# Kernel tuning notes

Measured on AMD Instinct MI355X. Metric: run time of the kernel, lower is better.

The kernel has to match this reference:

```python
import jax, jax.numpy as jnp
import numpy as np
import math

B, S, H, NH = 8, 1024, 1024, 16
DH = H // NH


def _ln(x, g, b, eps=1e-5):
    m = x.mean(-1, keepdims=True)
    v = ((x - m) ** 2).mean(-1, keepdims=True)
    return (x - m) / jnp.sqrt(v + eps) * g + b


def _attn(qx, kx, vx, wq, bq, wk, bk, wv, bv, wo, bo, mask):
    b = qx.shape[0]
    def heads(t, w, bias):
        return (t @ w + bias).reshape(b, -1, NH, DH).transpose(0, 2, 1, 3)
    q, k, v = heads(qx, wq, bq), heads(kx, wk, bk), heads(vx, wv, bv)
    corr = jnp.einsum('bhqd,bhkd->bhqk', q, k) / math.sqrt(DH)  # [B,NH,Sq,Sk]
    corr = jnp.where(mask[:, None, :, None] == 0, -1e9, corr)  # mask per query row
    p = jax.nn.softmax(corr, axis=-1)
    o = jnp.einsum('bhqk,bhkd->bhqd', p, v).transpose(0, 2, 1, 3).reshape(b, -1, H)
    return o @ wo + bo


def setup_inputs() -> dict:
    key = jax.random.key(0)
    ks = jax.random.split(key, 16)
    d = {}
    d['x'] = jax.random.normal(ks[0], (B, S, H), jnp.float32)
    d['h'] = jax.random.normal(ks[1], (B, S, H), jnp.float32)
    d['mask'] = jnp.ones((B, S), jnp.int32)
    wnames = ['sa_wq', 'sa_wk', 'sa_wv', 'sa_wo', 'ca_wq', 'ca_wk', 'ca_wv', 'ca_wo', 'ff_w1', 'ff_w2']
    for i, n in enumerate(wnames):
        d[n] = jax.random.normal(ks[2 + i], (H, H), jnp.float32) * 0.02
    for n in ['sa_bq', 'sa_bk', 'sa_bv', 'sa_bo', 'ca_bq', 'ca_bk', 'ca_bv', 'ca_bo', 'ff_b1', 'ff_b2']:
        d[n] = jnp.zeros((H,), jnp.float32)
    for n in ['ln1', 'ln2', 'ln3', 'lnh', 'ff_ln']:
        d[n + '_g'] = jnp.ones((H,), jnp.float32)
        d[n + '_b'] = jnp.zeros((H,), jnp.float32)
    return d


def reference(x, h, mask, ln1_g, ln1_b, ln2_g, ln2_b, ln3_g, ln3_b, lnh_g, lnh_b,
              sa_wq, sa_bq, sa_wk, sa_bk, sa_wv, sa_bv, sa_wo, sa_bo,
              ca_wq, ca_bq, ca_wk, ca_bk, ca_wv, ca_bv, ca_wo, ca_bo,
              ff_w1, ff_b1, ff_w2, ff_b2, ff_ln_g, ff_ln_b):
    # self-attention block (pre-LN, residual)
    xn = _ln(x, ln1_g, ln1_b)
    hidden_in = _attn(xn, xn, xn, sa_wq, sa_bq, sa_wk, sa_bk, sa_wv, sa_bv, sa_wo, sa_bo, mask) + x
    # cross-attention block
    mid_n = _ln(hidden_in, ln2_g, ln2_b)
    hn = _ln(h, lnh_g, lnh_b)
    hidden_mid = _attn(mid_n, hn, hn, ca_wq, ca_bq, ca_wk, ca_bk, ca_wv, ca_bv, ca_wo, ca_bo, mask) + hidden_in
    # position-wise FFN (Conv1d k=1 == pointwise linear) with its own LN+residual
    y = _ln(hidden_mid, ln3_g, ln3_b)
    ff = jax.nn.relu(y @ ff_w1 + ff_b1) @ ff_w2 + ff_b2
    ffo = _ln(ff + y, ff_ln_g, ff_ln_b)
    return ffo + hidden_mid
```

## Files before the change

kernel.cpp:

```cpp
#include <hip/hip_runtime.h>

typedef unsigned short u16;
typedef unsigned int u32;
typedef float f32x4 __attribute__((ext_vector_type(4)));
typedef float f32x16 __attribute__((ext_vector_type(16)));
typedef __bf16 bf16x8 __attribute__((ext_vector_type(8)));

#define MFMA16(a, b, c) __builtin_amdgcn_mfma_f32_16x16x32_bf16(a, b, c, 0, 0, 0)
#define MFMA32(a, b, c) __builtin_amdgcn_mfma_f32_32x32x16_bf16(a, b, c, 0, 0, 0)
#define PLSWAP(x, y) asm volatile("v_permlane32_swap_b32 %0, %1" : "+v"(x), "+v"(y))
#define CFENCE() asm volatile("" ::: "memory")
#define BAR()                         \
    {                                 \
        CFENCE();                     \
        __builtin_amdgcn_s_barrier(); \
        CFENCE();                     \
    }
#define WAITV(n) asm volatile("s_waitcnt vmcnt(" #n ")" ::: "memory")

__device__ __forceinline__ u16 f2b(float f) {
    u32 u = __builtin_bit_cast(u32, f);
    u += 0x7fffu + ((u >> 16) & 1u);
    return (u16)(u >> 16);
}

__device__ __forceinline__ float b2f(u16 v) {
    u32 u = ((u32)v) << 16;
    return __builtin_bit_cast(float, u);
}

__device__ __forceinline__ u32 pk2(float a, float b) {
    union { u32 u; __bf16 h[2]; } r;
    r.h[0] = (__bf16)a; r.h[1] = (__bf16)b;
    return r.u;
}

__device__ __forceinline__ void gload16(const u16* g, u16* l) {
    __builtin_amdgcn_global_load_lds((const __attribute__((address_space(1))) void*)g,
                                     (__attribute__((address_space(3))) void*)l, 16, 0, 0);
}

struct W10 { const float* p[10]; };
__global__ __launch_bounds__(256) void tcvt_k(W10 wp, u16* __restrict__ WT0) {
    const float* __restrict__ Wm = wp.p[blockIdx.z];
    u16* __restrict__ WT = WT0 + (size_t)blockIdx.z * 1048576;
    __shared__ float t[32][33];
    int bx = blockIdx.x, by = blockIdx.y;
    int tx = threadIdx.x, ty = threadIdx.y;
#pragma unroll
    for (int j = 0; j < 32; j += 8)
        t[ty + j][tx] = Wm[(size_t)(by * 32 + ty + j) * 1024 + bx * 32 + tx];
    __syncthreads();
#pragma unroll
    for (int j = 0; j < 32; j += 8)
        WT[(size_t)(bx * 32 + ty + j) * 1024 + by * 32 + tx] = f2b(t[tx][ty + j]);
}

template <int MODE>
__global__ __launch_bounds__(256) void ln_k(const float* __restrict__ in1, const float* __restrict__ in2,
                                            const float* __restrict__ gg, const float* __restrict__ bb,
                                            const float* __restrict__ post,
                                            float* __restrict__ of, u16* __restrict__ ob) {
    int row = blockIdx.x, tid = threadIdx.x;
    size_t base = (size_t)row * 1024 + tid * 4;
    float4 x = *(const float4*)(in1 + base);
    if constexpr (MODE & 1) {
        float4 x2 = *(const float4*)(in2 + base);
        x.x += x2.x; x.y += x2.y; x.z += x2.z; x.w += x2.w;
    }
    float s1 = x.x + x.y + x.z + x.w;
    float s2 = x.x * x.x + x.y * x.y + x.z * x.z + x.w * x.w;
#pragma unroll
    for (int m = 32; m >= 1; m >>= 1) { s1 += __shfl_xor(s1, m); s2 += __shfl_xor(s2, m); }
    __shared__ float r1[4], r2[4];
    int lane = tid & 63, w = tid >> 6;
    if (lane == 0) { r1[w] = s1; r2[w] = s2; }
    __syncthreads();
    s1 = r1[0] + r1[1] + r1[2] + r1[3];
    s2 = r2[0] + r2[1] + r2[2] + r2[3];
    float mean = s1 * (1.0f / 1024.0f);
    float var = s2 * (1.0f / 1024.0f) - mean * mean;
    float rstd = rsqrtf(var + 1e-5f);
    float4 gv = *(const float4*)(gg + tid * 4);
    float4 bv = *(const float4*)(bb + tid * 4);
    float y0 = (x.x - mean) * rstd * gv.x + bv.x;
    float y1 = (x.y - mean) * rstd * gv.y + bv.y;
    float y2 = (x.z - mean) * rstd * gv.z + bv.z;
    float y3 = (x.w - mean) * rstd * gv.w + bv.w;
    if constexpr (MODE & 2) {
        float o0 = y0, o1 = y1, o2 = y2, o3 = y3;
        if constexpr (MODE & 8) {
            float4 p = *(const float4*)(post + base);
            o0 += p.x; o1 += p.y; o2 += p.z; o3 += p.w;
        }
        float4 o; o.x = o0; o.y = o1; o.z = o2; o.w = o3;
        *(float4*)(of + base) = o;
    }
    if constexpr (MODE & 4) {
        uint2 pk;
        pk.x = (u32)f2b(y0) | ((u32)f2b(y1) << 16);
        pk.y = (u32)f2b(y2) | ((u32)f2b(y3) << 16);
        *(uint2*)(ob + base) = pk;
    }
}

__global__ __launch_bounds__(256) void ln2x_k(const float* __restrict__ inA, const float* __restrict__ gA,
                                              const float* __restrict__ bA, u16* __restrict__ obA,
                                              const float* __restrict__ inB, const float* __restrict__ gB,
                                              const float* __restrict__ bB, u16* __restrict__ obB) {
    int sel = blockIdx.x >> 13;
    int row = blockIdx.x & 8191;
    const float* in1 = sel ? inB : inA;
    const float* gg = sel ? gB : gA;
    const float* bb = sel ? bB : bA;
    u16* ob = sel ? obB : obA;
    int tid = threadIdx.x;
    size_t base = (size_t)row * 1024 + tid * 4;
    float4 x = *(const float4*)(in1 + base);
    float s1 = x.x + x.y + x.z + x.w;
    float s2 = x.x * x.x + x.y * x.y + x.z * x.z + x.w * x.w;
#pragma unroll
    for (int m = 32; m >= 1; m >>= 1) { s1 += __shfl_xor(s1, m); s2 += __shfl_xor(s2, m); }
    __shared__ float r1[4], r2[4];
    int lane = tid & 63, w = tid >> 6;
    if (lane == 0) { r1[w] = s1; r2[w] = s2; }
    __syncthreads();
    s1 = r1[0] + r1[1] + r1[2] + r1[3];
    s2 = r2[0] + r2[1] + r2[2] + r2[3];
    float mean = s1 * (1.0f / 1024.0f);
    float var = s2 * (1.0f / 1024.0f) - mean * mean;
    float rstd = rsqrtf(var + 1e-5f);
    float4 gv = *(const float4*)(gg + tid * 4);
    float4 bv = *(const float4*)(bb + tid * 4);
    uint2 pk;
    pk.x = pk2((x.x - mean) * rstd * gv.x + bv.x, (x.y - mean) * rstd * gv.y + bv.y);
    pk.y = pk2((x.z - mean) * rstd * gv.z + bv.z, (x.w - mean) * rstd * gv.w + bv.w);
    *(uint2*)(ob + base) = pk;
}

template <int EPI, int NBN, int VSEG>
__global__ __launch_bounds__(512) void gemm512_k(const u16* __restrict__ A, int lda,
                                                 const u16* __restrict__ WT,
                                                 const float* __restrict__ b0, const float* __restrict__ b1,
                                                 const float* __restrict__ b2,
                                                 float sc0, float sc1, float sc2,
                                                 const float* __restrict__ res,
                                                 void* __restrict__ outp, int ldc,
                                                 u16* __restrict__ vt) {
    constexpr int ASZ = 8192;
    constexpr int SLOT = ASZ + 4096;
    __shared__ u16 lds[3 * SLOT];
    u16* ldsb = &lds[0];

    int id = blockIdx.x;
    constexpr int NWG = 32 * NBN;
    constexpr int CPX = NWG / 8;
    int swz = (id & 7) * CPX + (id >> 3);
    int bm = swz / NBN, bn = swz % NBN;
    const int m0 = bm * 256, n0 = bn * 128;
    int tid = threadIdx.x, lane = tid & 63, w = tid >> 6;
    int col = lane & 15, fg = lane >> 4;
    int wr = w >> 1, wc = w & 1;

    int swzL = ((col * 32) + fg * 8) ^ ((col >> 1) << 3);
    int aoff0 = wr * 64 * 32 + swzL;
    int boff0 = ASZ + wc * 64 * 32 + swzL;

    int r = tid >> 2, g = tid & 3;
    int gr = r ^ ((r >> 3) & 1);
    int gc = g ^ ((r >> 1) & 3);
    const u16* pA = A + (size_t)(m0 + gr) * lda + gc * 8;
    const u16* pB = WT + (size_t)(n0 + gr) * 1024 + gc * 8;

#define STGA(t2, snO)                                                                       \
    {                                                                                       \
        gload16(pA + (size_t)(t2) * 32, ldsb + (snO) + w * 512);                            \
        gload16(pA + (size_t)(t2) * 32 + (size_t)128 * lda, ldsb + (snO) + 4096 + w * 512); \
    }
#define STGB(t2, snO)                                                   \
    {                                                                   \
        gload16(pB + (size_t)(t2) * 32, ldsb + (snO) + ASZ + w * 512);  \
    }

    f32x4 acc[4][4];
#pragma unroll
    for (int m = 0; m < 4; m++)
#pragma unroll
        for (int n = 0; n < 4; n++) acc[m][n] = (f32x4){0.f, 0.f, 0.f, 0.f};

    STGA(0, 0); STGB(0, 0);
    STGA(1, SLOT); STGB(1, SLOT);
    WAITV(3);
    BAR();

    int sc = 0, sn = 2;
    for (int t = 0; t < 32; ++t) {
        int sCur = sc * SLOT, sNxt = sn * SLOT;
        bf16x8 a0[4], bfv[2];
#pragma unroll
        for (int m = 0; m < 4; m++) a0[m] = *(const bf16x8*)&ldsb[sCur + aoff0 + m * 512];
#pragma unroll
        for (int n = 0; n < 2; n++) bfv[n] = *(const bf16x8*)&ldsb[sCur + boff0 + n * 512];
        if (t < 30) STGA(t + 2, sNxt);
        BAR();
        __builtin_amdgcn_s_setprio(1);
#pragma unroll
        for (int m = 0; m < 4; m++)
#pragma unroll
            for (int n = 0; n < 2; n++) acc[m][n] = MFMA16(a0[m], bfv[n], acc[m][n]);
        __builtin_amdgcn_s_setprio(0);
        BAR();
        bf16x8 b2[2];
#pragma unroll
        for (int n = 0; n < 2; n++) b2[n] = *(const bf16x8*)&ldsb[sCur + boff0 + (n + 2) * 512];
        if (t < 30) STGB(t + 2, sNxt);
        BAR();
        __builtin_amdgcn_s_setprio(1);
#pragma unroll
        for (int m = 0; m < 4; m++)
#pragma unroll
            for (int n = 0; n < 2; n++) acc[m][n + 2] = MFMA16(a0[m], b2[n], acc[m][n + 2]);
        __builtin_amdgcn_s_setprio(0);
        if (t < 30) { WAITV(3); } else if (t == 30) { WAITV(0); }
        BAR();
        sc = (sc == 2) ? 0 : sc + 1;
        sn = (sn == 2) ? 0 : sn + 1;
    }
#undef STGA
#undef STGB

    int seg = n0 >> 10;
    const float* bp = (seg == 0) ? b0 : (seg == 1 ? b1 : b2);
    float sg = (seg == 0) ? sc0 : (seg == 1 ? sc1 : sc2);
    int nseg = n0 & 1023;
    float bv[4];
#pragma unroll
    for (int n = 0; n < 4; n++) bv[n] = bp[nseg + wc * 64 + n * 16 + col];

    if constexpr (VSEG >= 0) {
        if (seg == VSEG) {
            int chl = wc * 64 + col;
            int keyl = wr * 64 + fg * 4;
#pragma unroll
            for (int m = 0; m < 4; m++)
#pragma unroll
                for (int n = 0; n < 4; n++) {
                    uint2 pk;
                    pk.x = pk2(acc[m][n][0] + bv[n], acc[m][n][1] + bv[n]);
                    pk.y = pk2(acc[m][n][2] + bv[n], acc[m][n][3] + bv[n]);
                    *(uint2*)&ldsb[(chl + n * 16) * 264 + keyl + m * 16] = pk;
                }
            BAR();
            int bidx = m0 >> 10;
            int keyg = m0 & 1023;
            int rowt = tid >> 5, cht = tid & 31;
#pragma unroll
            for (int p = 0; p < 8; p++) {
                int ch = p * 16 + rowt;
                uint4 v4 = *(const uint4*)&ldsb[ch * 264 + cht * 8];
                *(uint4*)(vt + ((size_t)(bidx * 1024 + nseg + ch) << 10) + keyg + cht * 8) = v4;
            }
            return;
        }
    }
#pragma unroll
    for (int m = 0; m < 4; m++) {
#pragma unroll
        for (int rr = 0; rr < 4; rr++) {
            int row = m0 + wr * 64 + m * 16 + fg * 4 + rr;
#pragma unroll
            for (int n = 0; n < 4; n++) {
                int c = n0 + wc * 64 + n * 16 + col;
                size_t idx = (size_t)row * ldc + c;
                float v = (acc[m][n][rr] + bv[n]) * sg;
                if constexpr (EPI == 0) ((u16*)outp)[idx] = f2b(v);
                else if constexpr (EPI == 1) ((u16*)outp)[idx] = f2b(fmaxf(v, 0.f));
                else if constexpr (EPI == 2) ((float*)outp)[idx] = v + res[idx];
            }
        }
    }
}

template <int EPI, int NBN>
__global__ __launch_bounds__(256) void gemm256_k(const u16* __restrict__ A, int lda,
                                                 const u16* __restrict__ WT,
                                                 const float* __restrict__ b0,
                                                 float sc0,
                                                 const void* __restrict__ res,
                                                 void* __restrict__ outp, int ldc) {
    constexpr int SLOT = 8192;
    __shared__ u16 lds[3 * SLOT];
    int id = blockIdx.x;
    constexpr int NWG = 64 * NBN;
    constexpr int CPX = NWG / 8;
    int swz = (id & 7) * CPX + (id >> 3);
    int bm = swz / NBN, bn = swz % NBN;
    const int m0 = bm * 128, n0 = bn * 128;
    int tid = threadIdx.x, lane = tid & 63, w = tid >> 6;
    int col = lane & 15, fg = lane >> 4;
    int wr = w >> 1, wc = w & 1;

    int swzL = ((col * 32) + fg * 8) ^ ((col >> 1) << 3);
    int aoff0 = wr * 64 * 32 + swzL;
    int boff0 = 4096 + wc * 64 * 32 + swzL;

    int r = tid >> 2, g = tid & 3;
    int gr = r ^ ((r >> 3) & 1);
    int gc = g ^ ((r >> 1) & 3);
    const u16* pA = A + (size_t)(m0 + gr) * lda + gc * 8;
    const u16* pB = WT + (size_t)(n0 + gr) * 1024 + gc * 8;

#define STG(t2, snO)                                                                              \
    {                                                                                             \
        gload16(pA + (size_t)(t2) * 32, lds + (snO) + w * 512);                                   \
        gload16(pA + (size_t)(t2) * 32 + (size_t)64 * lda, lds + (snO) + 2048 + w * 512);         \
        gload16(pB + (size_t)(t2) * 32, lds + (snO) + 4096 + w * 512);                            \
        gload16(pB + (size_t)(t2) * 32 + (size_t)64 * 1024, lds + (snO) + 4096 + 2048 + w * 512); \
    }

    f32x4 acc[4][4];
#pragma unroll
    for (int m = 0; m < 4; m++)
#pragma unroll
        for (int n = 0; n < 4; n++) acc[m][n] = (f32x4){0.f, 0.f, 0.f, 0.f};

    STG(0, 0);
    STG(1, SLOT);
    WAITV(4);
    BAR();

    int sc = 0, sn = 2;
    for (int t = 0; t < 32; ++t) {
        int sCur = sc * SLOT, sNxt = sn * SLOT;
        bf16x8 a0[4], bfv[4];
#pragma unroll
        for (int m = 0; m < 4; m++) a0[m] = *(const bf16x8*)&lds[sCur + aoff0 + m * 512];
#pragma unroll
        for (int n = 0; n < 4; n++) bfv[n] = *(const bf16x8*)&lds[sCur + boff0 + n * 512];
        if (t < 30) STG(t + 2, sNxt);
        BAR();
        __builtin_amdgcn_s_setprio(1);
#pragma unroll
        for (int m = 0; m < 4; m++)
#pragma unroll
            for (int n = 0; n < 4; n++) acc[m][n] = MFMA16(a0[m], bfv[n], acc[m][n]);
        __builtin_amdgcn_s_setprio(0);
        if (t < 30) { WAITV(4); } else if (t == 30) { WAITV(0); }
        BAR();
        sc = (sc == 2) ? 0 : sc + 1;
        sn = (sn == 2) ? 0 : sn + 1;
    }
#undef STG

    float bv[4];
#pragma unroll
    for (int n = 0; n < 4; n++) bv[n] = b0[(n0 & 1023) + wc * 64 + n * 16 + col];
#pragma unroll
    for (int m = 0; m < 4; m++) {
#pragma unroll
        for (int rr = 0; rr < 4; rr++) {
            int row = m0 + wr * 64 + m * 16 + fg * 4 + rr;
#pragma unroll
            for (int n = 0; n < 4; n++) {
                int c = n0 + wc * 64 + n * 16 + col;
                size_t idx = (size_t)row * ldc + c;
                float v = (acc[m][n][rr] + bv[n]) * sc0;
                if constexpr (EPI == 0) ((u16*)outp)[idx] = f2b(v);
                else if constexpr (EPI == 1) ((u16*)outp)[idx] = f2b(fmaxf(v, 0.f));
                else if constexpr (EPI == 2) ((float*)outp)[idx] = v + ((const float*)res)[idx];
                else if constexpr (EPI == 3) ((float*)outp)[idx] = v + b2f(((const u16*)res)[idx]);
            }
        }
    }
}

__global__ __launch_bounds__(512) void attn_k(const u16* __restrict__ Q, int ldq,
                                              const u16* __restrict__ Kc, int ldk,
                                              const u16* __restrict__ VT,
                                              const int* __restrict__ mask,
                                              u16* __restrict__ O, int ldo) {
    const int S = 1024;
    int gid = blockIdx.x;
    int bq = gid >> 7, hh = (gid >> 3) & 15, bb = gid & 7;
    int tid = threadIdx.x, lane = tid & 63, w = tid >> 6;
    int q = lane & 31, hl = lane >> 5;
    int q0w = bq * 256 + w * 32;

    __shared__ u16 sm[18432];
#define KT(b, r, c) sm[(b) * 9216 + (r) * 72 + (c)]
#define VTL(b, r, c) sm[(b) * 9216 + 4608 + (r) * 72 + (c)]

    const u16* Qrow = Q + ((size_t)bb * S + q0w + q) * ldq + hh * 64;
    bool mneg = (mask[bb * S + q0w + q] == 0);
    bf16x8 qf[4];
#pragma unroll
    for (int c = 0; c < 4; c++) {
        qf[c] = *(const bf16x8*)(Qrow + c * 16 + hl * 8);
        if (mneg) qf[c] = (bf16x8)(__bf16)0.f;
    }

    float l = 0.f;
    f32x16 oa[2];
#pragma unroll
    for (int i = 0; i < 16; i++) { oa[0][i] = 0.f; oa[1][i] = 0.f; }

    int kk = tid >> 3, ks = tid & 7;
    const u16* gK = Kc + ((size_t)bb * S + kk) * ldk + hh * 64 + ks * 8;
    const u16* gVT = VT + ((size_t)(bb * 16 + hh) * 64 + kk) * 1024 + ks * 8;
    uint4 kr0, vr0;

#define LOADT(t)                                              \
    {                                                         \
        kr0 = *(const uint4*)(gK + (size_t)(t) * 64 * ldk);   \
        vr0 = *(const uint4*)(gVT + (size_t)(t) * 64);        \
    }
#define STORET(bf)                            \
    {                                         \
        *(uint4*)&KT(bf, kk, ks * 8) = kr0;   \
        *(uint4*)&VTL(bf, kk, ks * 8) = vr0;  \
    }

    LOADT(0);
    STORET(0);

    for (int t = 0; t < 16; ++t) {
        int cur = t & 1;
        if (t < 15) LOADT(t + 1);
        __syncthreads();

        f32x16 sc[2];
#pragma unroll
        for (int i = 0; i < 16; i++) { sc[0][i] = 0.f; sc[1][i] = 0.f; }
        __builtin_amdgcn_s_setprio(1);
#pragma unroll
        for (int st = 0; st < 2; st++)
#pragma unroll
            for (int c = 0; c < 4; c++) {
                bf16x8 kf = *(const bf16x8*)&KT(cur, st * 32 + q, c * 16 + hl * 8);
                sc[st] = MFMA32(kf, qf[c], sc[st]);
            }
        __builtin_amdgcn_s_setprio(0);

#pragma unroll
        for (int st = 0; st < 2; st++)
#pragma unroll
            for (int rr = 0; rr < 16; rr++) sc[st][rr] = exp2f(sc[st][rr]);
        float ts[8];
#pragma unroll
        for (int i = 0; i < 8; i++)
            ts[i] = (sc[0][i] + sc[0][i + 8]) + (sc[1][i] + sc[1][i + 8]);
#pragma unroll
        for (int i = 0; i < 4; i++) ts[i] += ts[i + 4];
        l += (ts[0] + ts[2]) + (ts[1] + ts[3]);

        __builtin_amdgcn_s_setprio(1);
#pragma unroll
        for (int st = 0; st < 2; st++) {
            u32 wv[8];
#pragma unroll
            for (int j = 0; j < 8; j++) wv[j] = pk2(sc[st][2 * j], sc[st][2 * j + 1]);
            PLSWAP(wv[0], wv[2]); PLSWAP(wv[1], wv[3]);
            PLSWAP(wv[4], wv[6]); PLSWAP(wv[5], wv[7]);
#pragma unroll
            for (int c = 0; c < 2; c++) {
                union { u32 u[4]; bf16x8 v; } pb;
                pb.u[0] = wv[c * 4 + 0]; pb.u[1] = wv[c * 4 + 1];
                pb.u[2] = wv[c * 4 + 2]; pb.u[3] = wv[c * 4 + 3];
#pragma unroll
                for (int dd = 0; dd < 2; dd++) {
                    bf16x8 vf = *(const bf16x8*)&VTL(cur, dd * 32 + q, st * 32 + c * 16 + hl * 8);
                    oa[dd] = MFMA32(vf, pb.v, oa[dd]);
                }
            }
        }
        __builtin_amdgcn_s_setprio(0);

        if (t < 15) STORET(cur ^ 1);
    }

    l += __shfl_xor(l, 32);
    __syncthreads();
    float inv = 1.0f / l;
    u16* otw = sm + w * 2304;
#pragma unroll
    for (int dd = 0; dd < 2; dd++)
#pragma unroll
        for (int rr = 0; rr < 16; rr++) {
            int d = (rr & 3) + 8 * (rr >> 2) + 4 * hl + 32 * dd;
            otw[q * 72 + d] = f2b(oa[dd][rr] * inv);
        }
    __syncthreads();
    size_t obase = ((size_t)bb * S + q0w) * ldo + hh * 64;
#pragma unroll
    for (int i = 0; i < 4; i++) {
        int row = i * 8 + (lane >> 3);
        uint4 vdat = *(const uint4*)&otw[row * 72 + (lane & 7) * 8];
        *(uint4*)(O + obase + (size_t)row * ldo + (lane & 7) * 8) = vdat;
    }
#undef KT
#undef VTL
#undef LOADT
#undef STORET
}

extern "C" void kernel_launch(void* const* d_in, const int* in_sizes, int n_in,
                              void* d_out, int out_size, void* d_ws, size_t ws_size,
                              hipStream_t stream) {
    (void)in_sizes; (void)n_in; (void)out_size; (void)ws_size;
    const float* x = (const float*)d_in[0];
    const float* h = (const float*)d_in[1];
    const int* mask = (const int*)d_in[2];
    const float* W[10];
    const float* Bv[10];
    for (int i = 0; i < 10; i++) { W[i] = (const float*)d_in[3 + i]; Bv[i] = (const float*)d_in[13 + i]; }
    const float *ln1g = (const float*)d_in[23], *ln1b = (const float*)d_in[24];
    const float *ln2g = (const float*)d_in[25], *ln2b = (const float*)d_in[26];
    const float *ln3g = (const float*)d_in[27], *ln3b = (const float*)d_in[28];
    const float *lnhg = (const float*)d_in[29], *lnhb = (const float*)d_in[30];
    const float *flng = (const float*)d_in[31], *flnb = (const float*)d_in[32];

    const float SCLE = 0.18033688011112042f;

    char* ws = (char*)d_ws;
    size_t off = 0;
    auto alloc = [&](size_t bytes) -> char* {
        char* p = ws + off;
        off += (bytes + 255) & ~(size_t)255;
        return p;
    };
    const size_t MT = (size_t)8192 * 1024;
    u16* wtb = (u16*)alloc((size_t)10 * 1048576 * 2);
    u16* wt[10];
    for (int i = 0; i < 10; i++) wt[i] = wtb + (size_t)i * 1048576;
    u16* qkv = (u16*)alloc((size_t)8192 * 3072 * 2);
    u16* kv = qkv;
    u16* kb = qkv + (size_t)8192 * 2048;
    u16* bufA = (u16*)alloc(MT * 2);
    u16* qb   = (u16*)alloc(MT * 2);
    float* hid_in  = (float*)alloc(MT * 4);
    float* hid_mid = (float*)alloc(MT * 4);
    float* yf      = (float*)alloc(MT * 4);
    u16* hn = (u16*)yf;
    u16* vtb = (u16*)hid_mid;
    float* outF = (float*)d_out;

    W10 wp;
    for (int i = 0; i < 10; i++) wp.p[i] = W[i];
    tcvt_k<<<dim3(32, 32, 10), dim3(32, 8), 0, stream>>>(wp, wtb);

    ln_k<4><<<8192, 256, 0, stream>>>(x, nullptr, ln1g, ln1b, nullptr, nullptr, bufA);
    gemm512_k<0, 24, 2><<<768, 512, 0, stream>>>(bufA, 1024, wt[0], Bv[0], Bv[1], Bv[2], SCLE, 1.f, 1.f, nullptr, qkv, 3072, vtb);
    attn_k<<<512, 512, 0, stream>>>(qkv, 3072, qkv + 1024, 3072, vtb, mask, qkv, 3072);
    gemm256_k<2, 8><<<512, 256, 0, stream>>>(qkv, 3072, wt[3], Bv[3], 1.f, x, hid_in, 1024);

    ln2x_k<<<16384, 256, 0, stream>>>(hid_in, ln2g, ln2b, bufA, h, lnhg, lnhb, hn);
    gemm256_k<0, 8><<<512, 256, 0, stream>>>(bufA, 1024, wt[4], Bv[4], SCLE, nullptr, qb, 1024);
    gemm512_k<0, 16, 1><<<512, 512, 0, stream>>>(hn, 1024, wt[5], Bv[5], Bv[6], Bv[6], 1.f, 1.f, 1.f, nullptr, kv, 2048, vtb);
    attn_k<<<512, 512, 0, stream>>>(qb, 1024, kv, 2048, vtb, mask, qb, 1024);
    gemm256_k<2, 8><<<512, 256, 0, stream>>>(qb, 1024, wt[7], Bv[7], 1.f, hid_in, hid_mid, 1024);

    ln_k<4><<<8192, 256, 0, stream>>>(hid_mid, nullptr, ln3g, ln3b, nullptr, nullptr, bufA);
    gemm256_k<1, 8><<<512, 256, 0, stream>>>(bufA, 1024, wt[8], Bv[8], 1.f, nullptr, kb, 1024);
    gemm256_k<3, 8><<<512, 256, 0, stream>>>(kb, 1024, wt[9], Bv[9], 1.f, bufA, hid_in, 1024);
    ln_k<10><<<8192, 256, 0, stream>>>(hid_in, nullptr, flng, flnb, hid_mid, outF, nullptr);
}
```

Before: 418.8 us.

## Stage attention K/V tiles via direct global-to-LDS loads with XOR swizzle

The attention kernel's K and V^T tiles now go straight from global memory into shared memory through a gload16 helper (presumably buffer_load ... lds), replacing the register round-trip and explicit LDS store. The unpadded 64-wide LDS rows use an XOR swizzle on the column chunk to avoid bank conflicts, which also shrinks the buffer footprint. The next tile's load is issued right after the barrier so it overlaps compute. Correctness depends on gload16 completion being ordered by the existing barrier and waits, so there is a risk of a race if the wait on the async loads is missing.

```diff
diff --git a/kernel.cpp b/kernel.cpp
--- a/kernel.cpp
+++ b/kernel.cpp
@@ -387,8 +387,6 @@
     int q0w = bq * 256 + w * 32;
 
     __shared__ u16 sm[18432];
-#define KT(b, r, c) sm[(b) * 9216 + (r) * 72 + (c)]
-#define VTL(b, r, c) sm[(b) * 9216 + 4608 + (r) * 72 + (c)]
 
     const u16* Qrow = Q + ((size_t)bb * S + q0w + q) * ldq + hh * 64;
     bool mneg = (mask[bb * S + q0w + q] == 0);
@@ -404,29 +402,24 @@
 #pragma unroll
     for (int i = 0; i < 16; i++) { oa[0][i] = 0.f; oa[1][i] = 0.f; }
 
-    int kk = tid >> 3, ks = tid & 7;
-    const u16* gK = Kc + ((size_t)bb * S + kk) * ldk + hh * 64 + ks * 8;
-    const u16* gVT = VT + ((size_t)(bb * 16 + hh) * 64 + kk) * 1024 + ks * 8;
-    uint4 kr0, vr0;
-
-#define LOADT(t)                                              \
-    {                                                         \
-        kr0 = *(const uint4*)(gK + (size_t)(t) * 64 * ldk);   \
-        vr0 = *(const uint4*)(gVT + (size_t)(t) * 64);        \
-    }
-#define STORET(bf)                            \
-    {                                         \
-        *(uint4*)&KT(bf, kk, ks * 8) = kr0;   \
-        *(uint4*)&VTL(bf, kk, ks * 8) = vr0;  \
-    }
-
-    LOADT(0);
-    STORET(0);
+    int gr = w * 8 + (lane >> 3);
+    int gcs = (lane & 7) ^ (gr & 7);
+    const u16* gK = Kc + ((size_t)bb * S + gr) * ldk + hh * 64 + gcs * 8;
+    const u16* gVT = VT + ((size_t)(bb * 16 + hh) * 64 + gr) * 1024 + gcs * 8;
+    int cxor = (q & 7) << 3;
+
+#define STAGE(t, b)                                                  \
+    {                                                                \
+        gload16(gK + (size_t)(t) * 64 * ldk, sm + (b) * 8192 + w * 512);        \
+        gload16(gVT + (size_t)(t) * 64, sm + (b) * 8192 + 4096 + w * 512);      \
+    }
+
+    STAGE(0, 0);
 
     for (int t = 0; t < 16; ++t) {
         int cur = t & 1;
-        if (t < 15) LOADT(t + 1);
         __syncthreads();
+        if (t < 15) STAGE(t + 1, cur ^ 1);
 
         f32x16 sc[2];
 #pragma unroll
@@ -436,7 +429,8 @@
         for (int st = 0; st < 2; st++)
 #pragma unroll
             for (int c = 0; c < 4; c++) {
-                bf16x8 kf = *(const bf16x8*)&KT(cur, st * 32 + q, c * 16 + hl * 8);
+                bf16x8 kf = *(const bf16x8*)&sm[cur * 8192 + (st * 32 + q) * 64 +
+                                                ((c * 16 + hl * 8) ^ cxor)];
                 sc[st] = MFMA32(kf, qf[c], sc[st]);
             }
         __builtin_amdgcn_s_setprio(0);
@@ -468,15 +462,15 @@
                 pb.u[2] = wv[c * 4 + 2]; pb.u[3] = wv[c * 4 + 3];
 #pragma unroll
                 for (int dd = 0; dd < 2; dd++) {
-                    bf16x8 vf = *(const bf16x8*)&VTL(cur, dd * 32 + q, st * 32 + c * 16 + hl * 8);
+                    bf16x8 vf = *(const bf16x8*)&sm[cur * 8192 + 4096 + (dd * 32 + q) * 64 +
+                                                    ((st * 32 + c * 16 + hl * 8) ^ cxor)];
                     oa[dd] = MFMA32(vf, pb.v, oa[dd]);
                 }
             }
         }
         __builtin_amdgcn_s_setprio(0);
-
-        if (t < 15) STORET(cur ^ 1);
-    }
+    }
+#undef STAGE
 
     l += __shfl_xor(l, 32);
     __syncthreads();
@@ -497,10 +491,6 @@
         uint4 vdat = *(const uint4*)&otw[row * 72 + (lane & 7) * 8];
         *(uint4*)(O + obase + (size_t)row * ldo + (lane & 7) * 8) = vdat;
     }
-#undef KT
-#undef VTL
-#undef LOADT
-#undef STORET
 }
 
 extern "C" void kernel_launch(void* const* d_in, const int* in_sizes, int n_in,
```

Result: no change. 421.1 us (+0.5%).
